# Kernel optimization log

Hardware: AMD Instinct MI355X
Metric: run time of the kernel (lower is better)

The kernel has to match this reference:

```python
import jax, jax.numpy as jnp
import numpy as np

HEADS = 16
HD = 64
LN_EPS = 1e-5


def swish(x):
    return x * jax.nn.sigmoid(x)


def layer_norm(x):
    mu = jnp.mean(x, axis=-1, keepdims=True)
    var = jnp.var(x, axis=-1, keepdims=True)
    return (x - mu) * jax.lax.rsqrt(var + LN_EPS)


def setup_inputs() -> dict:
    key = jax.random.key(0)
    ks = jax.random.split(key, 5)
    B, L, D = 4, 2048, 1024
    x = jax.random.normal(ks[0], (B, L, D), dtype=jnp.float32)
    W_fc = jax.random.normal(ks[1], (D, HEADS * HD * 3), dtype=jnp.float32) * (1.0 / np.sqrt(D))
    b_fc = jax.random.normal(ks[2], (HEADS * HD * 3,), dtype=jnp.float32) * 0.01
    W_fc2 = jax.random.normal(ks[3], (HEADS * HD, D), dtype=jnp.float32) * (1.0 / np.sqrt(HEADS * HD))
    b_fc2 = jax.random.normal(ks[4], (D,), dtype=jnp.float32) * 0.01
    return {"x": x, "W_fc": W_fc, "b_fc": b_fc, "W_fc2": W_fc2, "b_fc2": b_fc2}


def reference(x, W_fc, b_fc, W_fc2, b_fc2):
    B, L, D = x.shape
    # fused QKV projection with swish activation (dropout is identity in eval)
    qkv = swish(jnp.einsum('bld,de->ble', x, W_fc) + b_fc)
    qkv = qkv.reshape(B, L, HEADS, 3 * HD)
    q, k, v = jnp.split(qkv, 3, axis=-1)  # each [B, L, H, hd]
    # NOTE: original scales by sqrt(length), not sqrt(hd)
    scores = jnp.einsum('bwhd,bmhd->bhwm', q, k) / jnp.sqrt(jnp.float32(L))
    att = jax.nn.softmax(scores, axis=-1)  # [B, H, L, L]
    new_v = jnp.einsum('bhwm,bmhd->bwhd', att, v).reshape(B, L, HEADS * HD)
    m = swish(jnp.einsum('ble,ed->bld', new_v, W_fc2) + b_fc2)
    return layer_norm(x + m)
```

## Files before the change

### kernel.cpp

```cpp
#include <hip/hip_runtime.h>
#include <cstddef>
#include <cstdint>

typedef unsigned short u16;
typedef __attribute__((ext_vector_type(8))) short short8;
typedef __attribute__((ext_vector_type(4))) float floatx4;

#define C1_SCALE 0.031882111f
#define LOG2E    1.4426950408889634f

__device__ __forceinline__ u16 f2bf(float f) {
    union { float f; unsigned int i; } v; v.f = f;
    unsigned int b = v.i;
    b += 0x7FFFu + ((b >> 16) & 1u);
    return (u16)(b >> 16);
}

__device__ __forceinline__ unsigned pk2bf(float lo, float hi) {
#if __has_builtin(__builtin_amdgcn_cvt_pk_bf16_f32)
    auto v = __builtin_amdgcn_cvt_pk_bf16_f32(lo, hi);
    union { decltype(v) b; unsigned u; } c; c.b = v; return c.u;
#else
    return (unsigned)f2bf(lo) | ((unsigned)f2bf(hi) << 16);
#endif
}
__device__ __forceinline__ int4 pack8bf(float4 a, float4 b) {
    union { unsigned u[4]; int4 v; } c;
    c.u[0] = pk2bf(a.x, a.y); c.u[1] = pk2bf(a.z, a.w);
    c.u[2] = pk2bf(b.x, b.y); c.u[3] = pk2bf(b.z, b.w);
    return c.v;
}
__device__ __forceinline__ float fastrcp(float x) {
#if __has_builtin(__builtin_amdgcn_rcpf)
    return __builtin_amdgcn_rcpf(x);
#else
    return 1.0f / x;
#endif
}
__device__ __forceinline__ float swishf(float s) {
    float e = __builtin_amdgcn_exp2f(-s * LOG2E);
    return s * fastrcp(1.0f + e);
}
__device__ __forceinline__ void glds16(const void* g, void* l) {
    __builtin_amdgcn_global_load_lds(
        (const __attribute__((address_space(1))) void*)g,
        (__attribute__((address_space(3))) void*)l, 16, 0, 0);
}

__global__ __launch_bounds__(256) void cast_kernel(
    const float* __restrict__ x, u16* __restrict__ xb)
{
    const size_t i = ((size_t)blockIdx.x * 256 + threadIdx.x) * 8;
    float4 a = *(const float4*)&x[i];
    float4 b = *(const float4*)&x[i + 4];
    *(int4*)&xb[i] = pack8bf(a, b);
}

__global__ __launch_bounds__(256) void transpose_kernel(
    const float* __restrict__ src, u16* __restrict__ dst, int R, int C)
{
    __shared__ u16 t[32][33];
    const int tx = threadIdx.x & 31, ty = threadIdx.x >> 5;
    const int r0 = blockIdx.y * 32, c0 = blockIdx.x * 32;
#pragma unroll
    for (int i = 0; i < 4; ++i)
        t[ty + i * 8][tx] = f2bf(src[(size_t)(r0 + ty + i * 8) * C + c0 + tx]);
    __syncthreads();
#pragma unroll
    for (int i = 0; i < 4; ++i)
        dst[(size_t)(c0 + ty + i * 8) * R + r0 + tx] = t[tx][ty + i * 8];
}

#define GEMM_STAGE(AP, BP, Kdim)                                              \
    {                                                                          \
        _Pragma("unroll")                                                      \
        for (int i = 0; i < 4; ++i) {                                          \
            const int row = i * 32 + (tid >> 3);                               \
            const int gp  = (tid & 7) ^ (row & 7);                             \
            glds16(&AP[(size_t)(row0 + row) * Kdim + k0 + gp * 8],             \
                   &As[i * 32 + wid * 8][0]);                                  \
            glds16(&BP[(size_t)(col0 + row) * Kdim + k0 + gp * 8],             \
                   &Bs[i * 32 + wid * 8][0]);                                  \
        }                                                                      \
    }

#define GEMM_COMPUTE()                                                         \
    {                                                                          \
        _Pragma("unroll")                                                      \
        for (int kc = 0; kc < 2; ++kc) {                                       \
            short8 af[4], bf[4];                                               \
            const int gl = ((kc * 4 + quad) ^ (l16 & 7)) * 8;                  \
            _Pragma("unroll")                                                  \
            for (int mt = 0; mt < 4; ++mt)                                     \
                af[mt] = *(const short8*)&As[wm * 64 + mt * 16 + l16][gl];     \
            _Pragma("unroll")                                                  \
            for (int nt = 0; nt < 4; ++nt)                                     \
                bf[nt] = *(const short8*)&Bs[wn * 64 + nt * 16 + l16][gl];     \
            _Pragma("unroll")                                                  \
            for (int mt = 0; mt < 4; ++mt)                                     \
                _Pragma("unroll")                                              \
                for (int nt = 0; nt < 4; ++nt)                                 \
                    acc[mt][nt] = __builtin_amdgcn_mfma_f32_16x16x32_bf16(     \
                        af[mt], bf[nt], acc[mt][nt], 0, 0, 0);                 \
        }                                                                      \
    }

__global__ __launch_bounds__(256) void gemm_qkv_kernel(
    const u16* __restrict__ A, const u16* __restrict__ BT,
    const float* __restrict__ bias, u16* __restrict__ qk, u16* __restrict__ vT)
{
    const int K = 1024;
    const int tid  = threadIdx.x;
    const int wid  = tid >> 6;
    const int lane = tid & 63;
    const int quad = lane >> 4;
    const int l16  = lane & 15;
    const int wm = wid >> 1, wn = wid & 1;
    const int row0 = blockIdx.y * 128, col0 = blockIdx.x * 128;

    __shared__ __align__(16) u16 As[128][64];
    __shared__ __align__(16) u16 Bs[128][64];

    floatx4 acc[4][4] = {};

    for (int k0 = 0; k0 < K; k0 += 64) {
        if (k0) __syncthreads();
        GEMM_STAGE(A, BT, K);
        __syncthreads();
        GEMM_COMPUTE();
    }

    float bb[4];
#pragma unroll
    for (int nt = 0; nt < 4; ++nt)
        bb[nt] = bias[col0 + wn * 64 + nt * 16 + l16];

    const int b = row0 >> 11;
#pragma unroll
    for (int mt = 0; mt < 4; ++mt) {
        const int rbase = row0 + wm * 64 + mt * 16 + quad * 4;
        const int l0 = rbase & 2047;
#pragma unroll
        for (int nt = 0; nt < 4; ++nt) {
            const int c = col0 + wn * 64 + nt * 16 + l16;
            const unsigned h = (unsigned)c / 192u;
            const int w = c - (int)h * 192;
            float sw[4];
#pragma unroll
            for (int r = 0; r < 4; ++r)
                sw[r] = swishf(acc[mt][nt][r] + bb[nt]);
            if (w < 128) {
                const float scl = (w >= 64) ? C1_SCALE : 1.0f;
#pragma unroll
                for (int r = 0; r < 4; ++r)
                    qk[(size_t)(rbase + r) * 2048 + h * 128 + w] = f2bf(sw[r] * scl);
            } else {
                union { unsigned u[2]; uint2 v; } pk;
                pk.u[0] = pk2bf(sw[0], sw[1]);
                pk.u[1] = pk2bf(sw[2], sw[3]);
                *(uint2*)&vT[(size_t)((b * 16 + (int)h) * 64 + (w - 128)) * 2048 + l0] = pk.v;
            }
        }
    }
}

__global__ __launch_bounds__(256) void gemm_out_kernel(
    const u16* __restrict__ A, const u16* __restrict__ BT,
    const float* __restrict__ bias, const float* __restrict__ xres,
    float* __restrict__ out)
{
    const int K = 1024, N = 1024;
    const int tid  = threadIdx.x;
    const int wid  = tid >> 6;
    const int lane = tid & 63;
    const int quad = lane >> 4;
    const int l16  = lane & 15;
    const int wm = wid >> 1, wn = wid & 1;
    const int row0 = blockIdx.y * 128, col0 = blockIdx.x * 128;

    __shared__ __align__(16) u16 As[128][64];
    __shared__ __align__(16) u16 Bs[128][64];

    floatx4 acc[4][4] = {};

    for (int k0 = 0; k0 < K; k0 += 64) {
        if (k0) __syncthreads();
        GEMM_STAGE(A, BT, K);
        __syncthreads();
        GEMM_COMPUTE();
    }

    float bb[4];
#pragma unroll
    for (int nt = 0; nt < 4; ++nt)
        bb[nt] = bias[col0 + wn * 64 + nt * 16 + l16];

#pragma unroll
    for (int mt = 0; mt < 4; ++mt) {
#pragma unroll
        for (int nt = 0; nt < 4; ++nt) {
#pragma unroll
            for (int r = 0; r < 4; ++r) {
                int row = row0 + wm * 64 + mt * 16 + quad * 4 + r;
                int col = col0 + wn * 64 + nt * 16 + l16;
                float sw = swishf(acc[mt][nt][r] + bb[nt]);
                out[(size_t)row * N + col] = xres[(size_t)row * N + col] + sw;
            }
        }
    }
}

__global__ __launch_bounds__(256) void attn_kernel(
    const u16* __restrict__ qk, const u16* __restrict__ vT,
    u16* __restrict__ newv)
{
    const int tid  = threadIdx.x;
    const int wid  = tid >> 6;
    const int lane = tid & 63;
    const int quad = lane >> 4;
    const int l16  = lane & 15;
    const int id = blockIdx.x;
    const int qt = id >> 6;
    const int hb = id & 63;
    const int h  = hb & 15;
    const int b  = hb >> 4;

    const u16* qkb = qk + (size_t)b * 2048 * 2048;
    const u16* vTb = vT + (size_t)(b * 16 + h) * 64 * 2048;

    short8 qf[2][2];
#pragma unroll
    for (int it = 0; it < 2; ++it) {
        const int qrow = qt * 128 + (wid * 2 + it) * 16 + l16;
        const u16* qp = &qkb[(size_t)qrow * 2048 + h * 128];
        qf[it][0] = *(const short8*)&qp[quad * 8];
        qf[it][1] = *(const short8*)&qp[32 + quad * 8];
    }

    const short one = (short)0x3F80;
    const short8 ones = {one, one, one, one, one, one, one, one};

    __shared__ __align__(16) u16 Ks[64][64];
    __shared__ __align__(16) u16 Vt[64][64];
    __shared__ __align__(16) u16 Ps[4][2][16][72];

    floatx4 oacc[2][4] = {};
    floatx4 sumacc[2] = {};

    for (int kt = 0; kt < 32; ++kt) {
        const int k0 = kt * 64;
        if (kt) __syncthreads();
#pragma unroll
        for (int i = 0; i < 2; ++i) {
            const int row = i * 32 + (tid >> 3);
            const int gp  = (tid & 7) ^ (row & 7);
            glds16(&qkb[(size_t)(k0 + row) * 2048 + h * 128 + 64 + gp * 8],
                   &Ks[i * 32 + wid * 8][0]);
            glds16(&vTb[(size_t)row * 2048 + k0 + gp * 8],
                   &Vt[i * 32 + wid * 8][0]);
        }
        __syncthreads();

        floatx4 sacc[2][4] = {};
#pragma unroll
        for (int kc = 0; kc < 2; ++kc) {
            const int gl = ((kc * 4 + quad) ^ (l16 & 7)) * 8;
#pragma unroll
            for (int nt = 0; nt < 4; ++nt) {
                short8 kf = *(const short8*)&Ks[nt * 16 + l16][gl];
                sacc[0][nt] = __builtin_amdgcn_mfma_f32_16x16x32_bf16(kf, qf[0][kc], sacc[0][nt], 0, 0, 0);
                sacc[1][nt] = __builtin_amdgcn_mfma_f32_16x16x32_bf16(kf, qf[1][kc], sacc[1][nt], 0, 0, 0);
            }
        }

#pragma unroll
        for (int it = 0; it < 2; ++it) {
#pragma unroll
            for (int nt = 0; nt < 4; ++nt) {
                float p0 = __builtin_amdgcn_exp2f(sacc[it][nt][0]);
                float p1 = __builtin_amdgcn_exp2f(sacc[it][nt][1]);
                float p2 = __builtin_amdgcn_exp2f(sacc[it][nt][2]);
                float p3 = __builtin_amdgcn_exp2f(sacc[it][nt][3]);
                union { unsigned u[2]; uint2 v; } pk;
                pk.u[0] = pk2bf(p0, p1);
                pk.u[1] = pk2bf(p2, p3);
                *(uint2*)&Ps[wid][it][l16][nt * 16 + quad * 4] = pk.v;
            }
        }

#pragma unroll
        for (int kc = 0; kc < 2; ++kc) {
            const int gl = ((kc * 4 + quad) ^ (l16 & 7)) * 8;
            short8 pf0 = *(const short8*)&Ps[wid][0][l16][kc * 32 + quad * 8];
            short8 pf1 = *(const short8*)&Ps[wid][1][l16][kc * 32 + quad * 8];
            sumacc[0] = __builtin_amdgcn_mfma_f32_16x16x32_bf16(ones, pf0, sumacc[0], 0, 0, 0);
            sumacc[1] = __builtin_amdgcn_mfma_f32_16x16x32_bf16(ones, pf1, sumacc[1], 0, 0, 0);
#pragma unroll
            for (int nt = 0; nt < 4; ++nt) {
                short8 vf = *(const short8*)&Vt[nt * 16 + l16][gl];
                oacc[0][nt] = __builtin_amdgcn_mfma_f32_16x16x32_bf16(vf, pf0, oacc[0][nt], 0, 0, 0);
                oacc[1][nt] = __builtin_amdgcn_mfma_f32_16x16x32_bf16(vf, pf1, oacc[1][nt], 0, 0, 0);
            }
        }
    }

#pragma unroll
    for (int it = 0; it < 2; ++it) {
        const float inv = fastrcp(sumacc[it][0]);
        const int row = qt * 128 + (wid * 2 + it) * 16 + l16;
        u16* orow = &newv[((size_t)b * 2048 + row) * 1024 + h * 64];
#pragma unroll
        for (int nt = 0; nt < 4; ++nt) {
            union { unsigned u[2]; uint2 v; } pk;
            pk.u[0] = pk2bf(oacc[it][nt][0] * inv, oacc[it][nt][1] * inv);
            pk.u[1] = pk2bf(oacc[it][nt][2] * inv, oacc[it][nt][3] * inv);
            *(uint2*)&orow[nt * 16 + quad * 4] = pk.v;
        }
    }
}

__global__ __launch_bounds__(256) void ln_kernel(
    const float* __restrict__ y, float* __restrict__ out)
{
    const int row = blockIdx.x;
    const int tid = threadIdx.x;
    const float* yr = y + (size_t)row * 1024;
    float v[4];
    float s1 = 0.f, s2 = 0.f;
#pragma unroll
    for (int i = 0; i < 4; ++i) {
        v[i] = yr[tid + i * 256];
        s1 += v[i];
        s2 += v[i] * v[i];
    }
#pragma unroll
    for (int off = 1; off < 64; off <<= 1) {
        s1 += __shfl_xor(s1, off, 64);
        s2 += __shfl_xor(s2, off, 64);
    }
    __shared__ float red1[4], red2[4];
    const int wid = tid >> 6, lane = tid & 63;
    if (lane == 0) { red1[wid] = s1; red2[wid] = s2; }
    __syncthreads();
    s1 = red1[0] + red1[1] + red1[2] + red1[3];
    s2 = red2[0] + red2[1] + red2[2] + red2[3];
    const float mu   = s1 * (1.0f / 1024.0f);
    const float var  = s2 * (1.0f / 1024.0f) - mu * mu;
    const float rstd = rsqrtf(var + 1e-5f);
    float* orow = out + (size_t)row * 1024;
#pragma unroll
    for (int i = 0; i < 4; ++i)
        orow[tid + i * 256] = (v[i] - mu) * rstd;
}

extern "C" void kernel_launch(void* const* d_in, const int* in_sizes, int n_in,
                              void* d_out, int out_size, void* d_ws, size_t ws_size,
                              hipStream_t stream) {
    const float* x     = (const float*)d_in[0];
    const float* W_fc  = (const float*)d_in[1];
    const float* b_fc  = (const float*)d_in[2];
    const float* W_fc2 = (const float*)d_in[3];
    const float* b_fc2 = (const float*)d_in[4];
    float* out = (float*)d_out;

    char* ob = (char*)d_out;
    u16* WfcT  = (u16*)ob;
    u16* Wfc2T = (u16*)(ob + 6291456);
    u16* xbf   = (u16*)(ob + 8388608);
    u16* newv  = (u16*)(ob + 8388608);

    char* ws = (char*)d_ws;
    u16*   qk = (u16*)ws;
    u16*   vT = (u16*)(ws + 33554432);
    float* y  = (float*)ws;

    cast_kernel<<<dim3(4096), 256, 0, stream>>>(x, xbf);
    transpose_kernel<<<dim3(96, 32), 256, 0, stream>>>(W_fc, WfcT, 1024, 3072);
    transpose_kernel<<<dim3(32, 32), 256, 0, stream>>>(W_fc2, Wfc2T, 1024, 1024);

    gemm_qkv_kernel<<<dim3(24, 64), 256, 0, stream>>>(xbf, WfcT, b_fc, qk, vT);

    attn_kernel<<<dim3(1024), 256, 0, stream>>>(qk, vT, newv);

    gemm_out_kernel<<<dim3(8, 64), 256, 0, stream>>>(newv, Wfc2T, b_fc2, x, y);

    ln_kernel<<<dim3(8192), 256, 0, stream>>>(y, out);
}
```

Before: 301.6 us.

## Double-buffer K/V tiles in attention and XOR-swizzle the P buffer

Makes the K and V shared-memory tiles double-buffered, so the next tile's global-to-LDS load is issued before the current tile's MFMAs and one barrier per iteration is dropped. The P staging buffer shrinks to one 16x64 tile per wave, replacing the padded layout with an XOR swizzle, and the PV product now runs per row group. This doubles K/V LDS use, which may reduce occupancy, and reusing the single P buffer serializes the two row groups within each wave.

```diff
diff --git a/kernel.cpp b/kernel.cpp
--- a/kernel.cpp
+++ b/kernel.cpp
@@ -240,26 +240,39 @@
     const short one = (short)0x3F80;
     const short8 ones = {one, one, one, one, one, one, one, one};
 
-    __shared__ __align__(16) u16 Ks[64][64];
-    __shared__ __align__(16) u16 Vt[64][64];
-    __shared__ __align__(16) u16 Ps[4][2][16][72];
-
+    __shared__ __align__(16) u16 Ks[2][64][64];
+    __shared__ __align__(16) u16 Vt[2][64][64];
+    __shared__ __align__(16) u16 Ps[4][16][64];
+
+    const int srow = tid >> 3;
+    const int sg0  = (tid & 7) ^ (srow & 7);
     floatx4 oacc[2][4] = {};
     floatx4 sumacc[2] = {};
 
+#pragma unroll
+    for (int i = 0; i < 2; ++i) {
+        const int row = i * 32 + srow;
+        glds16(&qkb[(size_t)row * 2048 + h * 128 + 64 + sg0 * 8],
+               &Ks[0][i * 32 + wid * 8][0]);
+        glds16(&vTb[(size_t)row * 2048 + sg0 * 8],
+               &Vt[0][i * 32 + wid * 8][0]);
+    }
+
     for (int kt = 0; kt < 32; ++kt) {
-        const int k0 = kt * 64;
-        if (kt) __syncthreads();
-#pragma unroll
-        for (int i = 0; i < 2; ++i) {
-            const int row = i * 32 + (tid >> 3);
-            const int gp  = (tid & 7) ^ (row & 7);
-            glds16(&qkb[(size_t)(k0 + row) * 2048 + h * 128 + 64 + gp * 8],
-                   &Ks[i * 32 + wid * 8][0]);
-            glds16(&vTb[(size_t)row * 2048 + k0 + gp * 8],
-                   &Vt[i * 32 + wid * 8][0]);
-        }
+        const int cur = kt & 1;
         __syncthreads();
+
+        if (kt + 1 < 32) {
+            const int k0n = (kt + 1) * 64;
+#pragma unroll
+            for (int i = 0; i < 2; ++i) {
+                const int row = i * 32 + srow;
+                glds16(&qkb[(size_t)(k0n + row) * 2048 + h * 128 + 64 + sg0 * 8],
+                       &Ks[cur ^ 1][i * 32 + wid * 8][0]);
+                glds16(&vTb[(size_t)row * 2048 + k0n + sg0 * 8],
+                       &Vt[cur ^ 1][i * 32 + wid * 8][0]);
+            }
+        }
 
         floatx4 sacc[2][4] = {};
 #pragma unroll
@@ -267,7 +280,7 @@
             const int gl = ((kc * 4 + quad) ^ (l16 & 7)) * 8;
 #pragma unroll
             for (int nt = 0; nt < 4; ++nt) {
-                short8 kf = *(const short8*)&Ks[nt * 16 + l16][gl];
+                short8 kf = *(const short8*)&Ks[cur][nt * 16 + l16][gl];
                 sacc[0][nt] = __builtin_amdgcn_mfma_f32_16x16x32_bf16(kf, qf[0][kc], sacc[0][nt], 0, 0, 0);
                 sacc[1][nt] = __builtin_amdgcn_mfma_f32_16x16x32_bf16(kf, qf[1][kc], sacc[1][nt], 0, 0, 0);
             }
@@ -284,22 +297,19 @@
                 union { unsigned u[2]; uint2 v; } pk;
                 pk.u[0] = pk2bf(p0, p1);
                 pk.u[1] = pk2bf(p2, p3);
-                *(uint2*)&Ps[wid][it][l16][nt * 16 + quad * 4] = pk.v;
-            }
-        }
-
-#pragma unroll
-        for (int kc = 0; kc < 2; ++kc) {
-            const int gl = ((kc * 4 + quad) ^ (l16 & 7)) * 8;
-            short8 pf0 = *(const short8*)&Ps[wid][0][l16][kc * 32 + quad * 8];
-            short8 pf1 = *(const short8*)&Ps[wid][1][l16][kc * 32 + quad * 8];
-            sumacc[0] = __builtin_amdgcn_mfma_f32_16x16x32_bf16(ones, pf0, sumacc[0], 0, 0, 0);
-            sumacc[1] = __builtin_amdgcn_mfma_f32_16x16x32_bf16(ones, pf1, sumacc[1], 0, 0, 0);
-#pragma unroll
-            for (int nt = 0; nt < 4; ++nt) {
-                short8 vf = *(const short8*)&Vt[nt * 16 + l16][gl];
-                oacc[0][nt] = __builtin_amdgcn_mfma_f32_16x16x32_bf16(vf, pf0, oacc[0][nt], 0, 0, 0);
-                oacc[1][nt] = __builtin_amdgcn_mfma_f32_16x16x32_bf16(vf, pf1, oacc[1][nt], 0, 0, 0);
+                const int col = (((nt * 2 + (quad >> 1)) ^ (l16 & 7)) * 8) + (quad & 1) * 4;
+                *(uint2*)&Ps[wid][l16][col] = pk.v;
+            }
+#pragma unroll
+            for (int kc = 0; kc < 2; ++kc) {
+                const int gl = ((kc * 4 + quad) ^ (l16 & 7)) * 8;
+                short8 pf = *(const short8*)&Ps[wid][l16][gl];
+                sumacc[it] = __builtin_amdgcn_mfma_f32_16x16x32_bf16(ones, pf, sumacc[it], 0, 0, 0);
+#pragma unroll
+                for (int nt = 0; nt < 4; ++nt) {
+                    short8 vf = *(const short8*)&Vt[cur][nt * 16 + l16][gl];
+                    oacc[it][nt] = __builtin_amdgcn_mfma_f32_16x16x32_bf16(vf, pf, oacc[it][nt], 0, 0, 0);
+                }
             }
         }
     }
```

Measured after the change: 317.8 us. 1.05x slower.
